# Optimization experiments

Hardware: AMD Instinct MI355X
Metric: run time of the kernel (lower is better)

The kernel has to match this reference:

```python
import jax, jax.numpy as jnp
import numpy as np
import math

EMBED_DIM = 768
NUM_HEADS = 12
N_QUBITS = 96
D_K = N_QUBITS // NUM_HEADS


def setup_inputs() -> dict:
    key = jax.random.key(0)
    k1, k2, k3 = jax.random.split(key, 3)
    x = jax.random.normal(k1, (8, 1024, EMBED_DIM), dtype=jnp.float32)
    # trainable RY angles, one per qubit (tq.RY has_params init ~ uniform small)
    theta = jax.random.uniform(k2, (N_QUBITS,), dtype=jnp.float32, minval=-math.pi, maxval=math.pi)
    # combine_heads: nn.Linear(n_qubits, embed_dim, bias=False) -> weight [out, in]
    W_combine = jax.random.normal(k3, (EMBED_DIM, N_QUBITS), dtype=jnp.float32) / math.sqrt(N_QUBITS)
    return {"x": x, "theta": theta, "W_combine": W_combine}


def reference(x, theta, W_combine):
    B, S, _ = x.shape
    # Quantum circuit is unentangled: per wire i, RX(x_i) then RY(theta_i) on |0>,
    # <PauliZ> = cos(x_i) * cos(theta_i). Fully batched over (B, S).
    xs = x[..., :N_QUBITS]                      # [B, S, nq]
    q_vecs = jnp.cos(xs) * jnp.cos(theta)       # [B, S, nq]

    # split heads: [B, H, S, d_k]; q == k == v
    q = q_vecs.reshape(B, S, NUM_HEADS, D_K).transpose(0, 2, 1, 3)

    scores = jnp.einsum('bhsd,bhtd->bhst', q, q) / math.sqrt(D_K)  # [B,H,S,S]
    probs = jax.nn.softmax(scores, axis=-1)
    attn = jnp.einsum('bhst,bhtd->bhsd', probs, q)                 # [B,H,S,d_k]
    attn = attn.transpose(0, 2, 1, 3).reshape(B, S, N_QUBITS)
    return attn @ W_combine.T                                       # [B,S,embed_dim]
```

## Files before the change

kernel.cpp:

```cpp
#include <hip/hip_runtime.h>
#include <hip/hip_bf16.h>

#define SEQ 1024
#define DK 8
#define NH 12
#define BATCH 8
#define NQ 96
#define ED 768

typedef __attribute__((ext_vector_type(8))) _Float16 half8;
typedef __attribute__((ext_vector_type(2))) __fp16 fp16x2;
typedef __attribute__((ext_vector_type(4))) float floatx4;
typedef __attribute__((ext_vector_type(2))) unsigned uint2v;

__device__ __forceinline__ float fast_exp2(float x) {
#if __has_builtin(__builtin_amdgcn_exp2f)
    return __builtin_amdgcn_exp2f(x);
#else
    return exp2f(x);
#endif
}

__device__ __forceinline__ unsigned pkh(float lo, float hi) {
    union { fp16x2 h; unsigned u; } v;
    v.h = __builtin_amdgcn_cvt_pkrtz(lo, hi);
    return v.u;
}

__global__ __launch_bounds__(512) void attn_kernel(
    const float* __restrict__ x, const float* __restrict__ theta,
    _Float16* __restrict__ attn )
{
    __shared__ __align__(16) _Float16 qv[SEQ * DK];
    __shared__ __align__(16) _Float16 qvt[32 * 512];
    __shared__ __align__(16) _Float16 pt[8 * 576];

    const int chunk = blockIdx.x;
    const int h     = blockIdx.y;
    const int b     = blockIdx.z;
    const int tid   = threadIdx.x;

    const float SQS = 0.71419170f;

    float ct[8];
    #pragma unroll
    for (int k = 0; k < 8; ++k) ct[k] = __cosf(theta[h * DK + k]);

    #pragma unroll
    for (int it = 0; it < 2; ++it) {
        const int s = tid + it * 512;
        const float* xp = x + ((size_t)(b * SEQ + s)) * ED + h * DK;
        const float4 v0 = *(const float4*)xp;
        const float4 v1 = *(const float4*)(xp + 4);
        float q[8];
        q[0] = __cosf(v0.x) * ct[0]; q[1] = __cosf(v0.y) * ct[1];
        q[2] = __cosf(v0.z) * ct[2]; q[3] = __cosf(v0.w) * ct[3];
        q[4] = __cosf(v1.x) * ct[4]; q[5] = __cosf(v1.y) * ct[5];
        q[6] = __cosf(v1.z) * ct[6]; q[7] = __cosf(v1.w) * ct[7];
        union { half8 v; _Float16 e[8]; } row;
        #pragma unroll
        for (int k = 0; k < 8; ++k) row.e[k] = (_Float16)(q[k] * SQS);
        *(half8*)&qv[s * DK] = row.v;
        const int e0 = (s >> 5) * 512 + ((s >> 3) & 3) * 128 + (s & 7);
        #pragma unroll
        for (int k = 0; k < 8; ++k) qvt[e0 + k * 8] = (_Float16)q[k];
    }
    {
        const int ww = tid >> 4, qq = (tid >> 2) & 3, np = tid & 3;
        const int n0 = 8 + np * 2;
        const int e  = ww * 512 + qq * 128 + n0 * 8;
        #pragma unroll
        for (int j = 0; j < 8; ++j) { qvt[e + j] = (_Float16)0.0f; qvt[e + 8 + j] = (_Float16)0.0f; }
    }
    __syncthreads();

    const int w    = tid >> 6;
    const int lane = tid & 63;
    const int l15  = lane & 15;
    const int qt   = lane >> 4;
    const int m0w  = chunk * 256 + w * 32;

    _Float16* zp = &qvt[72];
    _Float16* myp = &pt[w * 576];

    const half8 bfm0 = *(const half8*)((qt == 0) ? &qv[(m0w + l15) * DK]      : zp);
    const half8 bfm1 = *(const half8*)((qt == 0) ? &qv[(m0w + 16 + l15) * DK] : zp);

    const _Float16* pa0 = (qt == 0) ? &qv[l15 * DK]        : zp;
    const _Float16* pa1 = (qt == 0) ? &qv[(16 + l15) * DK] : zp;
    const int ainc = (qt == 0) ? 32 * DK : 0;
    const _Float16* pv = &qvt[qt * 128 + l15 * 8];

    _Float16* pw0 = &myp[l15 * 36 + qt * 4];
    _Float16* pw1 = pw0 + 16;
    const _Float16* pr = &myp[l15 * 36 + qt * 8];

    floatx4 acc0 = {0.f, 0.f, 0.f, 0.f};
    floatx4 acc1 = {0.f, 0.f, 0.f, 0.f};
    float lacc0 = 0.f, lacc1 = 0.f;
    const floatx4 zc = {0.f, 0.f, 0.f, 0.f};

    #pragma unroll 2
    for (int win = 0; win < 32; ++win) {
        const half8 af0 = *(const half8*)pa0;  pa0 += ainc;
        const half8 af1 = *(const half8*)pa1;  pa1 += ainc;
        const half8 vf  = *(const half8*)pv;   pv += 512;

        {
            floatx4 d0 = __builtin_amdgcn_mfma_f32_16x16x32_f16(af0, bfm0, zc, 0, 0, 0);
            floatx4 d1 = __builtin_amdgcn_mfma_f32_16x16x32_f16(af1, bfm0, zc, 0, 0, 0);
            const float e00 = fast_exp2(d0[0]), e01 = fast_exp2(d0[1]);
            const float e02 = fast_exp2(d0[2]), e03 = fast_exp2(d0[3]);
            const float e10 = fast_exp2(d1[0]), e11 = fast_exp2(d1[1]);
            const float e12 = fast_exp2(d1[2]), e13 = fast_exp2(d1[3]);
            lacc0 += ((e00 + e01) + (e02 + e03)) + ((e10 + e11) + (e12 + e13));
            *(uint2v*)pw0 = (uint2v){pkh(e00, e01), pkh(e02, e03)};
            *(uint2v*)pw1 = (uint2v){pkh(e10, e11), pkh(e12, e13)};
            const half8 paf = *(const half8*)pr;
            acc0 = __builtin_amdgcn_mfma_f32_16x16x32_f16(paf, vf, acc0, 0, 0, 0);
        }
        {
            floatx4 d0 = __builtin_amdgcn_mfma_f32_16x16x32_f16(af0, bfm1, zc, 0, 0, 0);
            floatx4 d1 = __builtin_amdgcn_mfma_f32_16x16x32_f16(af1, bfm1, zc, 0, 0, 0);
            const float e00 = fast_exp2(d0[0]), e01 = fast_exp2(d0[1]);
            const float e02 = fast_exp2(d0[2]), e03 = fast_exp2(d0[3]);
            const float e10 = fast_exp2(d1[0]), e11 = fast_exp2(d1[1]);
            const float e12 = fast_exp2(d1[2]), e13 = fast_exp2(d1[3]);
            lacc1 += ((e00 + e01) + (e02 + e03)) + ((e10 + e11) + (e12 + e13));
            *(uint2v*)pw0 = (uint2v){pkh(e00, e01), pkh(e02, e03)};
            *(uint2v*)pw1 = (uint2v){pkh(e10, e11), pkh(e12, e13)};
            const half8 paf = *(const half8*)pr;
            acc1 = __builtin_amdgcn_mfma_f32_16x16x32_f16(paf, vf, acc1, 0, 0, 0);
        }
    }

    lacc0 += __shfl_xor(lacc0, 16);
    lacc0 += __shfl_xor(lacc0, 32);
    lacc1 += __shfl_xor(lacc1, 16);
    lacc1 += __shfl_xor(lacc1, 32);

    #pragma unroll
    for (int r = 0; r < 4; ++r) {
        const float lsum = __shfl(lacc0, qt * 4 + r);
        const float val  = acc0[r] * __builtin_amdgcn_rcpf(lsum);
        if (l15 < 8) {
            const int m = m0w + qt * 4 + r;
            attn[((size_t)(b * SEQ + m)) * NQ + h * DK + l15] = (_Float16)val;
        }
    }
    #pragma unroll
    for (int r = 0; r < 4; ++r) {
        const float lsum = __shfl(lacc1, qt * 4 + r);
        const float val  = acc1[r] * __builtin_amdgcn_rcpf(lsum);
        if (l15 < 8) {
            const int m = m0w + 16 + qt * 4 + r;
            attn[((size_t)(b * SEQ + m)) * NQ + h * DK + l15] = (_Float16)val;
        }
    }
}

__global__ __launch_bounds__(256) void wconv_kernel(
    const float* __restrict__ W, _Float16* __restrict__ Wh)
{
    const int i = blockIdx.x * 256 + threadIdx.x;
    const float4 v = ((const float4*)W)[i];
    union { unsigned u[2]; double d; } o;
    o.u[0] = pkh(v.x, v.y);
    o.u[1] = pkh(v.z, v.w);
    ((double*)Wh)[i] = o.d;
}

__global__ __launch_bounds__(256) void proj_kernel(
    const _Float16* __restrict__ attn, const _Float16* __restrict__ Wh,
    float* __restrict__ out)
{
    const int tid  = threadIdx.x;
    const int w    = tid >> 6;
    const int lane = tid & 63;
    const int l15  = lane & 15;
    const int quad = lane >> 4;

    const int m0 = blockIdx.y * 64 + w * 16;
    const int n0 = blockIdx.x * 64;

    const size_t abase = ((size_t)(m0 + l15)) * NQ + quad * 8;
    half8 af0 = *(const half8*)(attn + abase);
    half8 af1 = *(const half8*)(attn + abase + 32);
    half8 af2 = *(const half8*)(attn + abase + 64);

    floatx4 acc[4];
    #pragma unroll
    for (int c = 0; c < 4; ++c) acc[c] = (floatx4){0.f, 0.f, 0.f, 0.f};

    #pragma unroll
    for (int c = 0; c < 4; ++c) {
        const size_t bbase = ((size_t)(n0 + c * 16 + l15)) * NQ + quad * 8;
        half8 b0 = *(const half8*)(Wh + bbase);
        half8 b1 = *(const half8*)(Wh + bbase + 32);
        half8 b2 = *(const half8*)(Wh + bbase + 64);
        acc[c] = __builtin_amdgcn_mfma_f32_16x16x32_f16(af0, b0, acc[c], 0, 0, 0);
        acc[c] = __builtin_amdgcn_mfma_f32_16x16x32_f16(af1, b1, acc[c], 0, 0, 0);
        acc[c] = __builtin_amdgcn_mfma_f32_16x16x32_f16(af2, b2, acc[c], 0, 0, 0);
    }

    #pragma unroll
    for (int c = 0; c < 4; ++c)
        #pragma unroll
        for (int r = 0; r < 4; ++r)
            out[((size_t)(m0 + quad * 4 + r)) * ED + n0 + c * 16 + l15] = acc[c][r];
}

extern "C" void kernel_launch(void* const* d_in, const int* in_sizes, int n_in,
                              void* d_out, int out_size, void* d_ws, size_t ws_size,
                              hipStream_t stream) {
    const float* x     = (const float*)d_in[0];
    const float* theta = (const float*)d_in[1];
    const float* W     = (const float*)d_in[2];
    float* out = (float*)d_out;

    _Float16* attn = (_Float16*)d_ws;
    _Float16* Wh   = (_Float16*)((char*)d_ws + (size_t)BATCH * SEQ * NQ * 2);

    wconv_kernel<<<dim3(ED * NQ / 4 / 256), 256, 0, stream>>>(W, Wh);
    attn_kernel<<<dim3(4, NH, BATCH), 512, 0, stream>>>(x, theta, attn);
    proj_kernel<<<dim3(ED / 64, (BATCH * SEQ) / 64), 256, 0, stream>>>(attn, Wh, out);
}
```

Baseline: 127.1 us.

## Software-pipeline attention loop with double P buffers across windows

```diff
diff --git a/kernel.cpp b/kernel.cpp
--- a/kernel.cpp
+++ b/kernel.cpp
@@ -33,7 +33,7 @@
 {
     __shared__ __align__(16) _Float16 qv[SEQ * DK];
     __shared__ __align__(16) _Float16 qvt[32 * 512];
-    __shared__ __align__(16) _Float16 pt[8 * 576];
+    __shared__ __align__(16) _Float16 pt[16 * 576];
 
     const int chunk = blockIdx.x;
     const int h     = blockIdx.y;
@@ -81,7 +81,8 @@
     const int m0w  = chunk * 256 + w * 32;
 
     _Float16* zp = &qvt[72];
-    _Float16* myp = &pt[w * 576];
+    _Float16* myp0 = &pt[(w * 2 + 0) * 576];
+    _Float16* myp1 = &pt[(w * 2 + 1) * 576];
 
     const half8 bfm0 = *(const half8*)((qt == 0) ? &qv[(m0w + l15) * DK]      : zp);
     const half8 bfm1 = *(const half8*)((qt == 0) ? &qv[(m0w + 16 + l15) * DK] : zp);
@@ -91,21 +92,21 @@
     const int ainc = (qt == 0) ? 32 * DK : 0;
     const _Float16* pv = &qvt[qt * 128 + l15 * 8];
 
-    _Float16* pw0 = &myp[l15 * 36 + qt * 4];
-    _Float16* pw1 = pw0 + 16;
-    const _Float16* pr = &myp[l15 * 36 + qt * 8];
+    _Float16* pw0_0 = &myp0[l15 * 36 + qt * 4];
+    _Float16* pw1_0 = pw0_0 + 16;
+    const _Float16* pr_0 = &myp0[l15 * 36 + qt * 8];
+    _Float16* pw0_1 = &myp1[l15 * 36 + qt * 4];
+    _Float16* pw1_1 = pw0_1 + 16;
+    const _Float16* pr_1 = &myp1[l15 * 36 + qt * 8];
 
     floatx4 acc0 = {0.f, 0.f, 0.f, 0.f};
     floatx4 acc1 = {0.f, 0.f, 0.f, 0.f};
     float lacc0 = 0.f, lacc1 = 0.f;
     const floatx4 zc = {0.f, 0.f, 0.f, 0.f};
 
-    #pragma unroll 2
-    for (int win = 0; win < 32; ++win) {
+    {
         const half8 af0 = *(const half8*)pa0;  pa0 += ainc;
         const half8 af1 = *(const half8*)pa1;  pa1 += ainc;
-        const half8 vf  = *(const half8*)pv;   pv += 512;
-
         {
             floatx4 d0 = __builtin_amdgcn_mfma_f32_16x16x32_f16(af0, bfm0, zc, 0, 0, 0);
             floatx4 d1 = __builtin_amdgcn_mfma_f32_16x16x32_f16(af1, bfm0, zc, 0, 0, 0);
@@ -114,10 +115,8 @@
             const float e10 = fast_exp2(d1[0]), e11 = fast_exp2(d1[1]);
             const float e12 = fast_exp2(d1[2]), e13 = fast_exp2(d1[3]);
             lacc0 += ((e00 + e01) + (e02 + e03)) + ((e10 + e11) + (e12 + e13));
-            *(uint2v*)pw0 = (uint2v){pkh(e00, e01), pkh(e02, e03)};
-            *(uint2v*)pw1 = (uint2v){pkh(e10, e11), pkh(e12, e13)};
-            const half8 paf = *(const half8*)pr;
-            acc0 = __builtin_amdgcn_mfma_f32_16x16x32_f16(paf, vf, acc0, 0, 0, 0);
+            *(uint2v*)pw0_0 = (uint2v){pkh(e00, e01), pkh(e02, e03)};
+            *(uint2v*)pw1_0 = (uint2v){pkh(e10, e11), pkh(e12, e13)};
         }
         {
             floatx4 d0 = __builtin_amdgcn_mfma_f32_16x16x32_f16(af0, bfm1, zc, 0, 0, 0);
@@ -127,11 +126,54 @@
             const float e10 = fast_exp2(d1[0]), e11 = fast_exp2(d1[1]);
             const float e12 = fast_exp2(d1[2]), e13 = fast_exp2(d1[3]);
             lacc1 += ((e00 + e01) + (e02 + e03)) + ((e10 + e11) + (e12 + e13));
-            *(uint2v*)pw0 = (uint2v){pkh(e00, e01), pkh(e02, e03)};
-            *(uint2v*)pw1 = (uint2v){pkh(e10, e11), pkh(e12, e13)};
-            const half8 paf = *(const half8*)pr;
-            acc1 = __builtin_amdgcn_mfma_f32_16x16x32_f16(paf, vf, acc1, 0, 0, 0);
-        }
+            *(uint2v*)pw0_1 = (uint2v){pkh(e00, e01), pkh(e02, e03)};
+            *(uint2v*)pw1_1 = (uint2v){pkh(e10, e11), pkh(e12, e13)};
+        }
+    }
+
+    #pragma unroll 2
+    for (int win = 1; win < 32; ++win) {
+        const half8 paf0 = *(const half8*)pr_0;
+        const half8 paf1 = *(const half8*)pr_1;
+        const half8 vf   = *(const half8*)pv;   pv += 512;
+
+        const half8 af0 = *(const half8*)pa0;  pa0 += ainc;
+        const half8 af1 = *(const half8*)pa1;  pa1 += ainc;
+
+        acc0 = __builtin_amdgcn_mfma_f32_16x16x32_f16(paf0, vf, acc0, 0, 0, 0);
+        acc1 = __builtin_amdgcn_mfma_f32_16x16x32_f16(paf1, vf, acc1, 0, 0, 0);
+
+        floatx4 d00 = __builtin_amdgcn_mfma_f32_16x16x32_f16(af0, bfm0, zc, 0, 0, 0);
+        floatx4 d01 = __builtin_amdgcn_mfma_f32_16x16x32_f16(af1, bfm0, zc, 0, 0, 0);
+        floatx4 d10 = __builtin_amdgcn_mfma_f32_16x16x32_f16(af0, bfm1, zc, 0, 0, 0);
+        floatx4 d11 = __builtin_amdgcn_mfma_f32_16x16x32_f16(af1, bfm1, zc, 0, 0, 0);
+
+        {
+            const float e00 = fast_exp2(d00[0]), e01 = fast_exp2(d00[1]);
+            const float e02 = fast_exp2(d00[2]), e03 = fast_exp2(d00[3]);
+            const float e10 = fast_exp2(d01[0]), e11 = fast_exp2(d01[1]);
+            const float e12 = fast_exp2(d01[2]), e13 = fast_exp2(d01[3]);
+            lacc0 += ((e00 + e01) + (e02 + e03)) + ((e10 + e11) + (e12 + e13));
+            *(uint2v*)pw0_0 = (uint2v){pkh(e00, e01), pkh(e02, e03)};
+            *(uint2v*)pw1_0 = (uint2v){pkh(e10, e11), pkh(e12, e13)};
+        }
+        {
+            const float e00 = fast_exp2(d10[0]), e01 = fast_exp2(d10[1]);
+            const float e02 = fast_exp2(d10[2]), e03 = fast_exp2(d10[3]);
+            const float e10 = fast_exp2(d11[0]), e11 = fast_exp2(d11[1]);
+            const float e12 = fast_exp2(d11[2]), e13 = fast_exp2(d11[3]);
+            lacc1 += ((e00 + e01) + (e02 + e03)) + ((e10 + e11) + (e12 + e13));
+            *(uint2v*)pw0_1 = (uint2v){pkh(e00, e01), pkh(e02, e03)};
+            *(uint2v*)pw1_1 = (uint2v){pkh(e10, e11), pkh(e12, e13)};
+        }
+    }
+
+    {
+        const half8 paf0 = *(const half8*)pr_0;
+        const half8 paf1 = *(const half8*)pr_1;
+        const half8 vf   = *(const half8*)pv;
+        acc0 = __builtin_amdgcn_mfma_f32_16x16x32_f16(paf0, vf, acc0, 0, 0, 0);
+        acc1 = __builtin_amdgcn_mfma_f32_16x16x32_f16(paf1, vf, acc1, 0, 0, 0);
     }
 
     lacc0 += __shfl_xor(lacc0, 16);
```

Result: slower. 136.9 us (+7.8%).
